# Performance work log

Measured on AMD Instinct MI355X. Metric: run time of the kernel, lower is better.

Reference implementation:

```python
import jax, jax.numpy as jnp
import numpy as np
from jax import lax

B, H, W, C = 2, 256, 256, 180
WS, SH, NH = 8, 4, 6
HD = C // NH          # 30
N = WS * WS           # 64
NW = (H // WS) * (W // WS)
HID = 4 * C
SCALE = HD ** -0.5
EPS = 1e-5


def _rel_pos_index(ws):
    coords = np.stack(np.meshgrid(np.arange(ws), np.arange(ws), indexing='ij'))  # [2,ws,ws]
    cf = coords.reshape(2, -1)
    rel = (cf[:, :, None] - cf[:, None, :]).transpose(1, 2, 0)  # [N,N,2]
    rel[:, :, 0] += ws - 1
    rel[:, :, 1] += ws - 1
    rel[:, :, 0] *= 2 * ws - 1
    return rel.sum(-1)  # [N,N]


def _attn_mask(h, w, ws, sh):
    img = np.zeros((h, w))
    sl = (slice(0, -ws), slice(-ws, -sh), slice(-sh, None))
    cnt = 0
    for hs in sl:
        for wsl in sl:
            img[hs, wsl] = cnt
            cnt += 1
    mw = img.reshape(h // ws, ws, w // ws, ws).transpose(0, 2, 1, 3).reshape(-1, ws * ws)  # [nW,N]
    d = mw[:, None, :] - mw[:, :, None]  # [nW,N,N]
    return np.where(d != 0, -100.0, 0.0).astype(np.float32)


REL_IDX = jnp.asarray(_rel_pos_index(WS))          # [N,N] int
MASK = jnp.asarray(_attn_mask(H, W, WS, SH))       # [nW,N,N] float


def _ln(x, g, b):
    m = jnp.mean(x, -1, keepdims=True)
    v = jnp.mean((x - m) ** 2, -1, keepdims=True)
    return (x - m) * lax.rsqrt(v + EPS) * g + b


def _win_part(x):  # (B,H,W,C) -> (B*nW,N,C)
    x = x.reshape(B, H // WS, WS, W // WS, WS, C).transpose(0, 1, 3, 2, 4, 5)
    return x.reshape(-1, N, C)


def _win_rev(w):  # (B*nW,N,C) -> (B,H,W,C)
    x = w.reshape(B, H // WS, W // WS, WS, WS, C).transpose(0, 1, 3, 2, 4, 5)
    return x.reshape(B, H, W, C)


def setup_inputs() -> dict:
    key = jax.random.key(0)
    ks = jax.random.split(key, 8)
    s = 0.02
    return {
        'x': jax.random.normal(ks[0], (B, H * W, C), jnp.float32),
        'norm1_g': jnp.ones((C,), jnp.float32),
        'norm1_b': jnp.zeros((C,), jnp.float32),
        'qkv_w': jax.random.normal(ks[1], (C, 3 * C), jnp.float32) * s,
        'qkv_b': jnp.zeros((3 * C,), jnp.float32),
        'rel_pos_table': jax.random.normal(ks[2], ((2 * WS - 1) ** 2, NH), jnp.float32) * s,
        'proj_w': jax.random.normal(ks[3], (C, C), jnp.float32) * s,
        'proj_b': jnp.zeros((C,), jnp.float32),
        'norm2_g': jnp.ones((C,), jnp.float32),
        'norm2_b': jnp.zeros((C,), jnp.float32),
        'fc1_w': jax.random.normal(ks[4], (C, HID), jnp.float32) * s,
        'fc1_b': jnp.zeros((HID,), jnp.float32),
        'dw_w': jax.random.normal(ks[5], (HID, 1, 3, 3), jnp.float32) * s,
        'dw_b': jnp.zeros((HID,), jnp.float32),
        'fc2_w': jax.random.normal(ks[6], (HID, C), jnp.float32) * s,
        'fc2_b': jnp.zeros((C,), jnp.float32),
    }


def reference(x, norm1_g, norm1_b, qkv_w, qkv_b, rel_pos_table, proj_w, proj_b,
              norm2_g, norm2_b, fc1_w, fc1_b, dw_w, dw_b, fc2_w, fc2_b):
    shortcut = x
    h = _ln(x, norm1_g, norm1_b).reshape(B, H, W, C)
    h = jnp.roll(h, (-SH, -SH), axis=(1, 2))           # cyclic shift
    xw = _win_part(h)                                   # [B*nW, N, C]

    qkv = (xw @ qkv_w + qkv_b).reshape(-1, N, 3, NH, HD).transpose(2, 0, 3, 1, 4)
    q, k, v = qkv[0] * SCALE, qkv[1], qkv[2]            # [B_,NH,N,HD]
    attn = jnp.einsum('bhnd,bhmd->bhnm', q, k)          # [B_,NH,N,N]

    bias = rel_pos_table[REL_IDX.reshape(-1)].reshape(N, N, NH).transpose(2, 0, 1)
    attn = attn + bias[None]
    attn = attn.reshape(B, NW, NH, N, N) + MASK[None, :, None]
    attn = jax.nn.softmax(attn.reshape(-1, NH, N, N), axis=-1)

    out = jnp.einsum('bhnm,bhmd->bhnd', attn, v).transpose(0, 2, 1, 3).reshape(-1, N, C)
    out = out @ proj_w + proj_b
    out = jnp.roll(_win_rev(out), (SH, SH), axis=(1, 2)).reshape(B, H * W, C)
    x = shortcut + out

    # MLP with depthwise-conv interleave
    m = _ln(x, norm2_g, norm2_b)
    m = jax.nn.gelu(m @ fc1_w + fc1_b, approximate=False)   # [B,L,HID]
    mc = m.transpose(0, 2, 1).reshape(B, HID, H, W)
    mc = lax.conv_general_dilated(mc, dw_w, (1, 1), 'SAME',
                                  feature_group_count=HID,
                                  dimension_numbers=('NCHW', 'OIHW', 'NCHW'))
    mc = mc + dw_b[None, :, None, None]
    m = jax.nn.gelu(mc.reshape(B, HID, H * W).transpose(0, 2, 1), approximate=False)
    m = m @ fc2_w + fc2_b
    return x + m
```

## Files before the change

kernel.cpp:

```cpp
#include <hip/hip_runtime.h>
#include <hip/hip_bf16.h>


using short8 = __attribute__((ext_vector_type(8))) short;
using f32x4  = __attribute__((ext_vector_type(4))) float;

constexpr int   ROWS   = 131072;
constexpr float SCALE_ = 0.18257418583505536f;

constexpr size_t OFF_WQ    = 0;
constexpr size_t OFF_WP    = OFF_WQ   + 576*192*2;
constexpr size_t OFF_WF1   = OFF_WP   + 192*192*2;
constexpr size_t OFF_WF2T  = OFF_WF1  + 768*192*2;
constexpr size_t OFF_BQ    = OFF_WF2T + 192*768*2;
constexpr size_t OFF_BP    = OFF_BQ   + 576*4;
constexpr size_t OFF_BF1   = OFF_BP   + 192*4;
constexpr size_t OFF_BF2   = OFF_BF1  + 768*4;
constexpr size_t OFF_BIASF = OFF_BF2  + 192*4;
constexpr size_t OFF_WDWT  = OFF_BIASF + 6*4096*4;
constexpr size_t OFF_BDW   = OFF_WDWT + 9*768*4;
constexpr size_t OFF_R1    = 1048576;
constexpr size_t SZ_R      = (size_t)ROWS * 192 * 2;
constexpr size_t OFF_R2    = OFF_R1 + SZ_R;
constexpr size_t OFF_R3    = OFF_R2 + SZ_R;
constexpr size_t WS_NEEDED = OFF_R3 + SZ_R;
static_assert(OFF_BDW + 768*4 <= OFF_R1, "weights overlap R1");
static_assert((size_t)66*256*768*2 <= SZ_R, "m1 band overflows R2");

__device__ __forceinline__ unsigned short f2bf(float f) {
    __hip_bfloat16 h = __float2bfloat16(f);
    return *reinterpret_cast<unsigned short*>(&h);
}
__device__ __forceinline__ float bf2f(unsigned short u) {
    union { unsigned int i; float f; } x; x.i = ((unsigned int)u) << 16; return x.f;
}
__device__ __forceinline__ float gelu_f(float x) {
    return 0.5f * x * (1.0f + erff(x * 0.70710678118654752f));
}

__global__ __launch_bounds__(256) void prep_kernel(
    const float* __restrict__ qkv_w, const float* __restrict__ qkv_b,
    const float* __restrict__ proj_w, const float* __restrict__ proj_b,
    const float* __restrict__ fc1_w, const float* __restrict__ fc1_b,
    const float* __restrict__ fc2_w, const float* __restrict__ fc2_b,
    const float* __restrict__ rpt,
    const float* __restrict__ dw_w, const float* __restrict__ dw_b,
    unsigned short* __restrict__ wq, unsigned short* __restrict__ wp,
    unsigned short* __restrict__ wf1, unsigned short* __restrict__ wf2t,
    float* __restrict__ bq, float* __restrict__ bp,
    float* __restrict__ bf1, float* __restrict__ bf2,
    float* __restrict__ biasf,
    float* __restrict__ wdwT, float* __restrict__ bdw)
{
    int idx = blockIdx.x * 256 + threadIdx.x;
    constexpr int E1 = 576*192;
    constexpr int E2 = E1 + 192*192;
    constexpr int E3 = E2 + 768*192;
    constexpr int E4 = E3 + 192*768;
    constexpr int E5 = E4 + 576;
    constexpr int E6 = E5 + 192;
    constexpr int E7 = E6 + 768;
    constexpr int E8 = E7 + 192;
    constexpr int E9 = E8 + 6*4096;
    constexpr int E10 = E9 + 9*768;
    constexpr int E11 = E10 + 768;
    if (idx < E1) {
        int n = idx / 192, kx = idx % 192;
        float v = 0.f;
        if (n < 540 && kx < 180) { v = qkv_w[kx*540 + n]; if (n < 180) v *= SCALE_; }
        wq[idx] = f2bf(v);
    } else if (idx < E2) {
        int j = idx - E1; int n = j / 192, kx = j % 192;
        wp[j] = f2bf((n < 180 && kx < 180) ? proj_w[kx*180 + n] : 0.f);
    } else if (idx < E3) {
        int j = idx - E2; int n = j / 192, kx = j % 192;
        wf1[j] = f2bf((n < 720 && kx < 180) ? fc1_w[kx*720 + n] : 0.f);
    } else if (idx < E4) {
        int j = idx - E3; int n = j / 768, kx = j % 768;
        wf2t[j] = f2bf((n < 180 && kx < 720) ? fc2_w[kx*180 + n] : 0.f);
    } else if (idx < E5) {
        int n = idx - E4;
        float v = (n < 540) ? qkv_b[n] : 0.f; if (n < 180) v *= SCALE_;
        bq[n] = v;
    } else if (idx < E6) {
        int n = idx - E5; bp[n] = (n < 180) ? proj_b[n] : 0.f;
    } else if (idx < E7) {
        int n = idx - E6; bf1[n] = (n < 720) ? fc1_b[n] : 0.f;
    } else if (idx < E8) {
        int n = idx - E7; bf2[n] = (n < 180) ? fc2_b[n] : 0.f;
    } else if (idx < E9) {
        int j = idx - E8;
        int hh = j / 4096, t = j & 4095;
        int n = t >> 6, m = t & 63;
        int rid = ((n>>3) - (m>>3) + 7)*15 + ((n&7) - (m&7) + 7);
        biasf[j] = rpt[rid*6 + hh];
    } else if (idx < E10) {
        int j = idx - E9;
        int tap = j / 768, c = j % 768;
        wdwT[j] = (c < 720) ? dw_w[c*9 + tap] : 0.f;
    } else if (idx < E11) {
        int c = idx - E10;
        bdw[c] = (c < 720) ? dw_b[c] : 0.f;
    }
}

template<int ROLL>
__global__ __launch_bounds__(256) void ln_kernel(const float* __restrict__ x,
    const float* __restrict__ g, const float* __restrict__ bsh,
    unsigned short* __restrict__ out)
{
    int row  = blockIdx.x * 4 + (threadIdx.x >> 6);
    int lane = threadIdx.x & 63;
    size_t src;
    if (ROLL) {
        int b    = row >> 16;
        int widx = (row >> 6) & 1023;
        int n    = row & 63;
        int hr   = ((widx >> 5) << 3) + (n >> 3);
        int wr   = ((widx & 31) << 3) + (n & 7);
        int h2   = (hr + 4) & 255;
        int w2   = (wr + 4) & 255;
        src = ((size_t)b << 16) + (h2 << 8) + w2;
    } else {
        src = (size_t)row;
    }
    const float* xr = x + src * 180;
    float v1 = xr[lane];
    float v2 = xr[lane + 64];
    float v3 = (lane < 52) ? xr[lane + 128] : 0.0f;
    float s1 = v1 + v2 + v3;
    float s2 = v1*v1 + v2*v2 + v3*v3;
    #pragma unroll
    for (int o = 32; o > 0; o >>= 1) { s1 += __shfl_xor(s1, o); s2 += __shfl_xor(s2, o); }
    float mean = s1 * (1.0f/180.0f);
    float var  = s2 * (1.0f/180.0f) - mean*mean;
    float rstd = rsqrtf(var + 1e-5f);
    unsigned short* orow = out + (size_t)row * 192;
    orow[lane]      = f2bf((v1 - mean)*rstd*g[lane]      + bsh[lane]);
    orow[lane + 64] = f2bf((v2 - mean)*rstd*g[lane + 64] + bsh[lane + 64]);
    if (lane < 52) orow[lane + 128] = f2bf((v3 - mean)*rstd*g[lane + 128] + bsh[lane + 128]);
    else           orow[lane + 128] = 0;
}

__global__ __launch_bounds__(256) void zeropad_kernel(unsigned int* q, unsigned int* k, unsigned int* v)
{
    int idx = blockIdx.x * 256 + threadIdx.x;
    int wid = idx / 192, t = idx % 192;
    if (t < 64)       q[wid*1024 + t*16 + 15] = 0;
    else if (t < 128) k[wid*1024 + (t-64)*16 + 15] = 0;
    else              v[wid*1024 + 960 + (t-128)] = 0;
}

template<int MODE>
__global__ __launch_bounds__(256) void gemm64(
    const unsigned short* __restrict__ A, const unsigned short* __restrict__ Bt,
    const float* __restrict__ bias, int K, int lda, int ldb, int ldo,
    float* __restrict__ out_f, const float* __restrict__ xres,
    unsigned short* __restrict__ oq, unsigned short* __restrict__ ok2,
    unsigned short* __restrict__ ov, unsigned short* __restrict__ obf)
{
    __shared__ __align__(16) unsigned short As[64*40];
    __shared__ __align__(16) unsigned short Bs[64*40];
    const int tid  = threadIdx.x;
    const int bm   = blockIdx.x, bn = blockIdx.y;
    const int lane = tid & 63;
    const int wv   = tid >> 6;
    const int wr   = wv >> 1, wc = wv & 1;
    const int l15  = lane & 15, l4 = lane >> 4;
    const int r    = tid >> 2;
    const int kk   = (tid & 3) << 3;

    f32x4 acc[2][2];
    #pragma unroll
    for (int i = 0; i < 2; i++)
        #pragma unroll
        for (int j = 0; j < 2; j++) acc[i][j] = f32x4{0.f, 0.f, 0.f, 0.f};

    const size_t abase = (size_t)(bm*64 + r) * (size_t)lda + kk;
    const size_t bbase = (size_t)(bn*64 + r) * (size_t)ldb + kk;
    const int lds_wi = r*40 + kk;

    for (int kt = 0; kt < K; kt += 32) {
        *(uint4*)&As[lds_wi] = *(const uint4*)&A[abase + kt];
        *(uint4*)&Bs[lds_wi] = *(const uint4*)&Bt[bbase + kt];
        __syncthreads();
        short8 af[2], bf[2];
        #pragma unroll
        for (int fm = 0; fm < 2; fm++) af[fm] = *(const short8*)&As[(wr*32 + fm*16 + l15)*40 + l4*8];
        #pragma unroll
        for (int fn = 0; fn < 2; fn++) bf[fn] = *(const short8*)&Bs[(wc*32 + fn*16 + l15)*40 + l4*8];
        #pragma unroll
        for (int fm = 0; fm < 2; fm++)
            #pragma unroll
            for (int fn = 0; fn < 2; fn++)
                acc[fm][fn] = __builtin_amdgcn_mfma_f32_16x16x32_bf16(af[fm], bf[fn], acc[fm][fn], 0, 0, 0);
        __syncthreads();
    }

    #pragma unroll
    for (int fm = 0; fm < 2; fm++) {
      #pragma unroll
      for (int fn = 0; fn < 2; fn++) {
        #pragma unroll
        for (int rr = 0; rr < 4; rr++) {
            int row_l = wr*32 + fm*16 + l4*4 + rr;
            int col_l = wc*32 + fn*16 + l15;
            int grow  = bm*64 + row_l;
            int gcol  = bn*64 + col_l;
            float v = acc[fm][fn][rr] + bias[gcol];
            if (MODE == 0) {
                if (gcol < 540) {
                    int which = (gcol >= 360) ? 2 : (gcol >= 180 ? 1 : 0);
                    int cc = gcol - which*180;
                    int hh = cc / 30;
                    int dd = cc - hh*30;
                    size_t wid = (size_t)(grow >> 6)*6 + hh;
                    if (which == 0)      oq [wid*2048 + (grow & 63)*32 + dd] = f2bf(v);
                    else if (which == 1) ok2[wid*2048 + (grow & 63)*32 + dd] = f2bf(v);
                    else                 ov [wid*2048 + dd*64 + (grow & 63)] = f2bf(v);
                }
            } else if (MODE == 1) {
                if (gcol < 180) {
                    int b    = grow >> 16;
                    int widx = (grow >> 6) & 1023;
                    int n    = grow & 63;
                    int hr   = ((widx >> 5) << 3) + (n >> 3);
                    int wr2  = ((widx & 31) << 3) + (n & 7);
                    int h2   = (hr + 4) & 255;
                    int w2   = (wr2 + 4) & 255;
                    size_t orow = ((size_t)b << 16) + (h2 << 8) + w2;
                    out_f[orow*180 + gcol] = xres[orow*180 + gcol] + v;
                }
            } else if (MODE == 2) {
                obf[(size_t)grow*ldo + gcol] = f2bf(gelu_f(v));
            } else {
                if (gcol < 180) out_f[(size_t)grow*180 + gcol] += v;
            }
        }
      }
    }
}

__global__ __launch_bounds__(64) void attn_kernel(
    const unsigned short* __restrict__ q, const unsigned short* __restrict__ k,
    const unsigned short* __restrict__ vt, const float* __restrict__ biasf,
    unsigned short* __restrict__ aout)
{
    __shared__ __align__(16) unsigned short P[64*72];
    const int wid  = blockIdx.x;
    const int b_   = wid / 6, hh = wid % 6;
    const int lane = threadIdx.x;
    const int l15  = lane & 15, l4 = lane >> 4;

    const unsigned short* qb = q  + (size_t)wid*2048;
    const unsigned short* kb = k  + (size_t)wid*2048;
    const unsigned short* vb = vt + (size_t)wid*2048;

    short8 qf[4], kf[4];
    #pragma unroll
    for (int t = 0; t < 4; t++) {
        qf[t] = *(const short8*)&qb[(t*16 + l15)*32 + l4*8];
        kf[t] = *(const short8*)&kb[(t*16 + l15)*32 + l4*8];
    }
    f32x4 s[4][4];
    #pragma unroll
    for (int m = 0; m < 4; m++)
        #pragma unroll
        for (int n = 0; n < 4; n++)
            s[m][n] = __builtin_amdgcn_mfma_f32_16x16x32_bf16(qf[m], kf[n], f32x4{0.f,0.f,0.f,0.f}, 0, 0, 0);

    const int wi = b_ & 1023;
    const int wh = wi >> 5, ww = wi & 31;
    const bool edge = (wh == 31) || (ww == 31);
    const float* bh = biasf + hh*4096;
    #pragma unroll
    for (int m = 0; m < 4; m++) {
      #pragma unroll
      for (int rr = 0; rr < 4; rr++) {
        int ni = m*16 + l4*4 + rr;
        int ln_n = 0;
        if (edge) {
            int rh = (wh < 31) ? 0 : (((ni >> 3) < 4) ? 1 : 2);
            int rw = (ww < 31) ? 0 : (((ni & 7) < 4) ? 1 : 2);
            ln_n = rh*3 + rw;
        }
        #pragma unroll
        for (int n = 0; n < 4; n++) {
            int mj = n*16 + l15;
            float add = bh[ni*64 + mj];
            if (edge) {
                int rh = (wh < 31) ? 0 : (((mj >> 3) < 4) ? 1 : 2);
                int rw = (ww < 31) ? 0 : (((mj & 7) < 4) ? 1 : 2);
                if (rh*3 + rw != ln_n) add -= 100.0f;
            }
            s[m][n][rr] += add;
        }
      }
    }
    #pragma unroll
    for (int m = 0; m < 4; m++) {
      #pragma unroll
      for (int rr = 0; rr < 4; rr++) {
        float mx = fmaxf(fmaxf(s[m][0][rr], s[m][1][rr]), fmaxf(s[m][2][rr], s[m][3][rr]));
        #pragma unroll
        for (int o = 8; o > 0; o >>= 1) mx = fmaxf(mx, __shfl_xor(mx, o));
        float sum = 0.f;
        #pragma unroll
        for (int n = 0; n < 4; n++) { float e = __expf(s[m][n][rr] - mx); s[m][n][rr] = e; sum += e; }
        #pragma unroll
        for (int o = 8; o > 0; o >>= 1) sum += __shfl_xor(sum, o);
        float inv = 1.0f / sum;
        int ni = m*16 + l4*4 + rr;
        #pragma unroll
        for (int n = 0; n < 4; n++) P[ni*72 + n*16 + l15] = f2bf(s[m][n][rr] * inv);
      }
    }
    __syncthreads();
    f32x4 po[4][2];
    #pragma unroll
    for (int m = 0; m < 4; m++)
        #pragma unroll
        for (int n = 0; n < 2; n++) po[m][n] = f32x4{0.f,0.f,0.f,0.f};
    #pragma unroll
    for (int ks = 0; ks < 2; ks++) {
        short8 pf[4], vf[2];
        #pragma unroll
        for (int m = 0; m < 4; m++) pf[m] = *(const short8*)&P[(m*16 + l15)*72 + ks*32 + l4*8];
        #pragma unroll
        for (int n = 0; n < 2; n++) vf[n] = *(const short8*)&vb[(n*16 + l15)*64 + ks*32 + l4*8];
        #pragma unroll
        for (int m = 0; m < 4; m++)
            #pragma unroll
            for (int n = 0; n < 2; n++)
                po[m][n] = __builtin_amdgcn_mfma_f32_16x16x32_bf16(pf[m], vf[n], po[m][n], 0, 0, 0);
    }
    #pragma unroll
    for (int m = 0; m < 4; m++)
      #pragma unroll
      for (int n = 0; n < 2; n++)
        #pragma unroll
        for (int rr = 0; rr < 4; rr++) {
            int ni = m*16 + l4*4 + rr;
            int dd = n*16 + l15;
            if (dd < 30)
                aout[((size_t)b_*64 + ni)*192 + hh*30 + dd] = f2bf(po[m][n][rr]);
        }
}

__global__ __launch_bounds__(256) void dwconv_band(
    const unsigned short* __restrict__ m1, const float* __restrict__ wT,
    const float* __restrict__ bias, int h0, unsigned short* __restrict__ m2)
{
    const int hl  = blockIdx.x;
    const int t   = threadIdx.x;
    const int cg  = t & 31;
    const int pl  = t >> 5;
    const int w0  = blockIdx.y * 64 + pl * 8;
    const int c   = blockIdx.z * 256 + cg * 8;

    float acc[8][8];
    float bv[8];
    *(f32x4*)&bv[0] = *(const f32x4*)&bias[c];
    *(f32x4*)&bv[4] = *(const f32x4*)&bias[c + 4];
    #pragma unroll
    for (int p = 0; p < 8; p++)
        #pragma unroll
        for (int i = 0; i < 8; i++) acc[p][i] = bv[i];

    const short8 zv = {0,0,0,0,0,0,0,0};
    #pragma unroll
    for (int dh = -1; dh <= 1; dh++) {
        int hg = h0 + hl + dh;
        if (hg < 0 || hg > 255) continue;
        const unsigned short* rb = m1 + (size_t)(hl + 1 + dh) * 256 * 768 + c;
        float f[10][8];
        #pragma unroll
        for (int j = 0; j < 10; j++) {
            int w2 = w0 - 1 + j;
            short8 v = (w2 < 0 || w2 > 255) ? zv : *(const short8*)&rb[(size_t)w2*768];
            #pragma unroll
            for (int i = 0; i < 8; i++) f[j][i] = bf2f((unsigned short)v[i]);
        }
        #pragma unroll
        for (int dw2 = 0; dw2 < 3; dw2++) {
            const float* wrow = wT + ((dh+1)*3 + dw2)*768 + c;
            float wt[8];
            *(f32x4*)&wt[0] = *(const f32x4*)&wrow[0];
            *(f32x4*)&wt[4] = *(const f32x4*)&wrow[4];
            #pragma unroll
            for (int p = 0; p < 8; p++)
                #pragma unroll
                for (int i = 0; i < 8; i++)
                    acc[p][i] += f[p + dw2][i] * wt[i];
        }
    }
    unsigned short* ob = m2 + ((size_t)hl*256 + w0)*768 + c;
    #pragma unroll
    for (int p = 0; p < 8; p++) {
        short8 o;
        #pragma unroll
        for (int i = 0; i < 8; i++) o[i] = (short)f2bf(gelu_f(acc[p][i]));
        *(short8*)&ob[(size_t)p*768] = o;
    }
}

extern "C" void kernel_launch(void* const* d_in, const int* in_sizes, int n_in,
                              void* d_out, int out_size, void* d_ws, size_t ws_size,
                              hipStream_t stream) {
    (void)in_sizes; (void)n_in; (void)out_size;
    if (ws_size < WS_NEEDED) return;
    const float* x      = (const float*)d_in[0];
    const float* n1g    = (const float*)d_in[1];
    const float* n1b    = (const float*)d_in[2];
    const float* qkv_w  = (const float*)d_in[3];
    const float* qkv_b  = (const float*)d_in[4];
    const float* rpt    = (const float*)d_in[5];
    const float* proj_w = (const float*)d_in[6];
    const float* proj_b = (const float*)d_in[7];
    const float* n2g    = (const float*)d_in[8];
    const float* n2b    = (const float*)d_in[9];
    const float* fc1_w  = (const float*)d_in[10];
    const float* fc1_b  = (const float*)d_in[11];
    const float* dw_w   = (const float*)d_in[12];
    const float* dw_b   = (const float*)d_in[13];
    const float* fc2_w  = (const float*)d_in[14];
    const float* fc2_b  = (const float*)d_in[15];
    float* out = (float*)d_out;
    char*  ws  = (char*)d_ws;

    unsigned short* wq   = (unsigned short*)(ws + OFF_WQ);
    unsigned short* wp   = (unsigned short*)(ws + OFF_WP);
    unsigned short* wf1  = (unsigned short*)(ws + OFF_WF1);
    unsigned short* wf2t = (unsigned short*)(ws + OFF_WF2T);
    float* bq    = (float*)(ws + OFF_BQ);
    float* bp    = (float*)(ws + OFF_BP);
    float* bf1   = (float*)(ws + OFF_BF1);
    float* bf2   = (float*)(ws + OFF_BF2);
    float* biasf = (float*)(ws + OFF_BIASF);
    float* wdwT  = (float*)(ws + OFF_WDWT);
    float* bdw   = (float*)(ws + OFF_BDW);
    unsigned short* R1 = (unsigned short*)(ws + OFF_R1);
    unsigned short* R2 = (unsigned short*)(ws + OFF_R2);
    unsigned short* R3 = (unsigned short*)(ws + OFF_R3);
    unsigned short* qp = (unsigned short*)d_out;

    prep_kernel<<<1861, 256, 0, stream>>>(qkv_w, qkv_b, proj_w, proj_b, fc1_w, fc1_b,
                                          fc2_w, fc2_b, rpt, dw_w, dw_b,
                                          wq, wp, wf1, wf2t,
                                          bq, bp, bf1, bf2, biasf, wdwT, bdw);
    ln_kernel<1><<<32768, 256, 0, stream>>>(x, n1g, n1b, R1);
    gemm64<0><<<dim3(2048, 9), 256, 0, stream>>>(R1, wq, bq, 192, 192, 192, 0,
                                                 nullptr, nullptr, qp, R2, R3, nullptr);
    zeropad_kernel<<<9216, 256, 0, stream>>>((unsigned int*)qp, (unsigned int*)R2, (unsigned int*)R3);
    attn_kernel<<<12288, 64, 0, stream>>>(qp, R2, R3, biasf, R1);
    gemm64<1><<<dim3(2048, 3), 256, 0, stream>>>(R1, wp, bp, 192, 192, 192, 0,
                                                 out, x, nullptr, nullptr, nullptr, nullptr);
    ln_kernel<0><<<32768, 256, 0, stream>>>(out, n2g, n2b, R1);
    for (int band = 0; band < 8; ++band) {
        const int b_img   = band >> 2;
        const int h0      = (band & 3) * 64;
        const int h_start = (h0 == 0) ? 0 : h0 - 1;
        const int h_end   = (h0 + 64 < 256) ? (h0 + 65) : 256;
        const int n_rows  = h_end - h_start;
        const int moff    = (h0 == 0) ? 1 : 0;
        const size_t arow0 = ((size_t)b_img*256 + h_start) * 256;
        const size_t pix0  = ((size_t)b_img*256 + h0) * 256;
        gemm64<2><<<dim3(n_rows*4, 12), 256, 0, stream>>>(
            R1 + arow0*192, wf1, bf1, 192, 192, 192, 768,
            nullptr, nullptr, nullptr, nullptr, nullptr, R2 + (size_t)moff*256*768);
        dwconv_band<<<dim3(64, 4, 3), 256, 0, stream>>>(R2, wdwT, bdw, h0, R3);
        gemm64<3><<<dim3(256, 3), 256, 0, stream>>>(
            R3, wf2t, bf2, 768, 768, 768, 0,
            out + pix0*180, nullptr, nullptr, nullptr, nullptr, nullptr);
    }
}
```

Baseline: 897.7 us.

## Fuse LN1, QKV GEMM, window attention and projection into one per-window kernel

Replaces the separate roll+LayerNorm, QKV GEMM, zero-pad, attention and projection kernels with one kernel per window. Each block holds the normalized tokens, Q/K/V, the probabilities and the attention output in LDS. This removes the global round trips for the bf16 intermediates and several launches. The cost is about 113KB of LDS and 384 threads per block, so only one block fits per CU. The QKV and projection weights are also read straight from global memory by every block.

```diff
diff --git a/kernel.cpp b/kernel.cpp
--- a/kernel.cpp
+++ b/kernel.cpp
@@ -104,27 +104,13 @@
     }
 }
 
-template<int ROLL>
 __global__ __launch_bounds__(256) void ln_kernel(const float* __restrict__ x,
     const float* __restrict__ g, const float* __restrict__ bsh,
     unsigned short* __restrict__ out)
 {
     int row  = blockIdx.x * 4 + (threadIdx.x >> 6);
     int lane = threadIdx.x & 63;
-    size_t src;
-    if (ROLL) {
-        int b    = row >> 16;
-        int widx = (row >> 6) & 1023;
-        int n    = row & 63;
-        int hr   = ((widx >> 5) << 3) + (n >> 3);
-        int wr   = ((widx & 31) << 3) + (n & 7);
-        int h2   = (hr + 4) & 255;
-        int w2   = (wr + 4) & 255;
-        src = ((size_t)b << 16) + (h2 << 8) + w2;
-    } else {
-        src = (size_t)row;
-    }
-    const float* xr = x + src * 180;
+    const float* xr = x + (size_t)row * 180;
     float v1 = xr[lane];
     float v2 = xr[lane + 64];
     float v3 = (lane < 52) ? xr[lane + 128] : 0.0f;
@@ -142,22 +128,249 @@
     else           orow[lane + 128] = 0;
 }
 
-__global__ __launch_bounds__(256) void zeropad_kernel(unsigned int* q, unsigned int* k, unsigned int* v)
+__global__ __launch_bounds__(384, 1) void fused_attn(
+    const float* __restrict__ x,
+    const float* __restrict__ n1g, const float* __restrict__ n1b,
+    const unsigned short* __restrict__ wq, const float* __restrict__ bq,
+    const unsigned short* __restrict__ wp, const float* __restrict__ bp,
+    const float* __restrict__ biasf, float* __restrict__ out)
 {
-    int idx = blockIdx.x * 256 + threadIdx.x;
-    int wid = idx / 192, t = idx % 192;
-    if (t < 64)       q[wid*1024 + t*16 + 15] = 0;
-    else if (t < 128) k[wid*1024 + (t-64)*16 + 15] = 0;
-    else              v[wid*1024 + 960 + (t-128)] = 0;
+    __shared__ __align__(16) char lds[115712];
+    unsigned short* xn  = (unsigned short*)(lds);
+    unsigned short* qs  = (unsigned short*)(lds + 26624);
+    unsigned short* ks  = (unsigned short*)(lds + 57344);
+    unsigned short* vsT = (unsigned short*)(lds + 88064);
+    unsigned short* P   = (unsigned short*)(lds);
+    unsigned short* ao  = (unsigned short*)(lds + 88064);
+
+    const int wid  = blockIdx.x;
+    const int b_   = wid >> 10;
+    const int wi   = wid & 1023;
+    const int wh   = wi >> 5, ww = wi & 31;
+    const int tid  = threadIdx.x;
+    const int wv   = tid >> 6;
+    const int lane = tid & 63;
+    const int l15  = lane & 15, l4 = lane >> 4;
+
+    for (int n = wv; n < 64; n += 6) {
+        int h2 = (wh*8 + (n >> 3) + 4) & 255;
+        int w2 = (ww*8 + (n & 7) + 4) & 255;
+        const float* xr = x + ((size_t)(b_ << 16) + (h2 << 8) + w2) * 180;
+        float v1 = xr[lane];
+        float v2 = xr[lane + 64];
+        float v3 = (lane < 52) ? xr[lane + 128] : 0.0f;
+        float s1 = v1 + v2 + v3;
+        float s2 = v1*v1 + v2*v2 + v3*v3;
+        #pragma unroll
+        for (int o = 32; o > 0; o >>= 1) { s1 += __shfl_xor(s1, o); s2 += __shfl_xor(s2, o); }
+        float mean = s1 * (1.0f/180.0f);
+        float var  = s2 * (1.0f/180.0f) - mean*mean;
+        float rstd = rsqrtf(var + 1e-5f);
+        unsigned short* orow = xn + n*208;
+        orow[lane]      = f2bf((v1 - mean)*rstd*n1g[lane]      + n1b[lane]);
+        orow[lane + 64] = f2bf((v2 - mean)*rstd*n1g[lane + 64] + n1b[lane + 64]);
+        if (lane < 52) orow[lane + 128] = f2bf((v3 - mean)*rstd*n1g[lane + 128] + n1b[lane + 128]);
+        else           orow[lane + 128] = 0;
+    }
+    {
+        int hh = tid >> 6, tk = tid & 63;
+        *(unsigned int*)&qs[(hh*64 + tk)*40 + 30] = 0;
+        *(unsigned int*)&ks[(hh*64 + tk)*40 + 30] = 0;
+    }
+    __syncthreads();
+
+    {
+        f32x4 acc[4][6];
+        #pragma unroll
+        for (int m = 0; m < 4; m++)
+            #pragma unroll
+            for (int nb = 0; nb < 6; nb++) acc[m][nb] = f32x4{0.f,0.f,0.f,0.f};
+        for (int kt = 0; kt < 6; kt++) {
+            short8 af[4];
+            #pragma unroll
+            for (int m = 0; m < 4; m++)
+                af[m] = *(const short8*)&xn[(m*16 + l15)*208 + kt*32 + l4*8];
+            #pragma unroll
+            for (int nb = 0; nb < 6; nb++) {
+                short8 bf = *(const short8*)&wq[(size_t)(wv*96 + nb*16 + l15)*192 + kt*32 + l4*8];
+                #pragma unroll
+                for (int m = 0; m < 4; m++)
+                    acc[m][nb] = __builtin_amdgcn_mfma_f32_16x16x32_bf16(af[m], bf, acc[m][nb], 0, 0, 0);
+            }
+        }
+        #pragma unroll
+        for (int m = 0; m < 4; m++) {
+          #pragma unroll
+          for (int nb = 0; nb < 6; nb++) {
+            #pragma unroll
+            for (int rr = 0; rr < 4; rr++) {
+                int tok  = m*16 + l4*4 + rr;
+                int gcol = wv*96 + nb*16 + l15;
+                if (gcol < 540) {
+                    float v = acc[m][nb][rr] + bq[gcol];
+                    int which = (gcol >= 360) ? 2 : (gcol >= 180 ? 1 : 0);
+                    int cc = gcol - which*180;
+                    int hh = cc / 30;
+                    int dd = cc - hh*30;
+                    if (which == 0)      qs [(hh*64 + tok)*40 + dd] = f2bf(v);
+                    else if (which == 1) ks [(hh*64 + tok)*40 + dd] = f2bf(v);
+                    else                 vsT[(hh*32 + dd)*72 + tok] = f2bf(v);
+                }
+            }
+          }
+        }
+    }
+    __syncthreads();
+
+    const int hh = wv;
+    f32x4 s[4][4];
+    {
+        short8 qf[4], kf[4];
+        #pragma unroll
+        for (int t = 0; t < 4; t++) {
+            qf[t] = *(const short8*)&qs[(hh*64 + t*16 + l15)*40 + l4*8];
+            kf[t] = *(const short8*)&ks[(hh*64 + t*16 + l15)*40 + l4*8];
+        }
+        #pragma unroll
+        for (int m = 0; m < 4; m++)
+            #pragma unroll
+            for (int n = 0; n < 4; n++)
+                s[m][n] = __builtin_amdgcn_mfma_f32_16x16x32_bf16(qf[m], kf[n], f32x4{0.f,0.f,0.f,0.f}, 0, 0, 0);
+    }
+    const bool edge = (wh == 31) || (ww == 31);
+    const float* bh = biasf + hh*4096;
+    #pragma unroll
+    for (int m = 0; m < 4; m++) {
+      #pragma unroll
+      for (int rr = 0; rr < 4; rr++) {
+        int ni = m*16 + l4*4 + rr;
+        int ln_n = 0;
+        if (edge) {
+            int rh = (wh < 31) ? 0 : (((ni >> 3) < 4) ? 1 : 2);
+            int rw = (ww < 31) ? 0 : (((ni & 7) < 4) ? 1 : 2);
+            ln_n = rh*3 + rw;
+        }
+        #pragma unroll
+        for (int n = 0; n < 4; n++) {
+            int mj = n*16 + l15;
+            float add = bh[ni*64 + mj];
+            if (edge) {
+                int rh = (wh < 31) ? 0 : (((mj >> 3) < 4) ? 1 : 2);
+                int rw = (ww < 31) ? 0 : (((mj & 7) < 4) ? 1 : 2);
+                if (rh*3 + rw != ln_n) add -= 100.0f;
+            }
+            s[m][n][rr] += add;
+        }
+      }
+    }
+    #pragma unroll
+    for (int m = 0; m < 4; m++) {
+      #pragma unroll
+      for (int rr = 0; rr < 4; rr++) {
+        float mx = fmaxf(fmaxf(s[m][0][rr], s[m][1][rr]), fmaxf(s[m][2][rr], s[m][3][rr]));
+        #pragma unroll
+        for (int o = 8; o > 0; o >>= 1) mx = fmaxf(mx, __shfl_xor(mx, o));
+        float sum = 0.f;
+        #pragma unroll
+        for (int n = 0; n < 4; n++) { float e = __expf(s[m][n][rr] - mx); s[m][n][rr] = e; sum += e; }
+        #pragma unroll
+        for (int o = 8; o > 0; o >>= 1) sum += __shfl_xor(sum, o);
+        float inv = 1.0f / sum;
+        #pragma unroll
+        for (int n = 0; n < 4; n++) s[m][n][rr] *= inv;
+      }
+    }
+    __syncthreads();
+
+    #pragma unroll
+    for (int m = 0; m < 4; m++)
+      #pragma unroll
+      for (int rr = 0; rr < 4; rr++) {
+        int ni = m*16 + l4*4 + rr;
+        #pragma unroll
+        for (int n = 0; n < 4; n++) P[(hh*64 + ni)*72 + n*16 + l15] = f2bf(s[m][n][rr]);
+      }
+    f32x4 po[4][2];
+    #pragma unroll
+    for (int m = 0; m < 4; m++)
+        #pragma unroll
+        for (int n = 0; n < 2; n++) po[m][n] = f32x4{0.f,0.f,0.f,0.f};
+    #pragma unroll
+    for (int ksx = 0; ksx < 2; ksx++) {
+        short8 pf[4], vf[2];
+        #pragma unroll
+        for (int m = 0; m < 4; m++) pf[m] = *(const short8*)&P[(hh*64 + m*16 + l15)*72 + ksx*32 + l4*8];
+        #pragma unroll
+        for (int n = 0; n < 2; n++) vf[n] = *(const short8*)&vsT[(hh*32 + n*16 + l15)*72 + ksx*32 + l4*8];
+        #pragma unroll
+        for (int m = 0; m < 4; m++)
+            #pragma unroll
+            for (int n = 0; n < 2; n++)
+                po[m][n] = __builtin_amdgcn_mfma_f32_16x16x32_bf16(pf[m], vf[n], po[m][n], 0, 0, 0);
+    }
+    __syncthreads();
+
+    #pragma unroll
+    for (int m = 0; m < 4; m++)
+      #pragma unroll
+      for (int n = 0; n < 2; n++)
+        #pragma unroll
+        for (int rr = 0; rr < 4; rr++) {
+            int tok = m*16 + l4*4 + rr;
+            int dd  = n*16 + l15;
+            if (dd < 30) ao[tok*208 + hh*30 + dd] = f2bf(po[m][n][rr]);
+        }
+    if (wv == 0) {
+        #pragma unroll
+        for (int c = 0; c < 6; c++)
+            *(unsigned int*)&ao[lane*208 + 180 + c*2] = 0;
+    }
+    __syncthreads();
+
+    {
+        f32x4 pacc[4][2];
+        #pragma unroll
+        for (int m = 0; m < 4; m++)
+            #pragma unroll
+            for (int nb = 0; nb < 2; nb++) pacc[m][nb] = f32x4{0.f,0.f,0.f,0.f};
+        for (int kt = 0; kt < 6; kt++) {
+            short8 paf[4];
+            #pragma unroll
+            for (int m = 0; m < 4; m++)
+                paf[m] = *(const short8*)&ao[(m*16 + l15)*208 + kt*32 + l4*8];
+            #pragma unroll
+            for (int nb = 0; nb < 2; nb++) {
+                short8 pbf = *(const short8*)&wp[(size_t)(wv*32 + nb*16 + l15)*192 + kt*32 + l4*8];
+                #pragma unroll
+                for (int m = 0; m < 4; m++)
+                    pacc[m][nb] = __builtin_amdgcn_mfma_f32_16x16x32_bf16(paf[m], pbf, pacc[m][nb], 0, 0, 0);
+            }
+        }
+        #pragma unroll
+        for (int m = 0; m < 4; m++) {
+          #pragma unroll
+          for (int nb = 0; nb < 2; nb++) {
+            int gcol = wv*32 + nb*16 + l15;
+            if (gcol < 180) {
+              #pragma unroll
+              for (int rr = 0; rr < 4; rr++) {
+                int tok = m*16 + l4*4 + rr;
+                int h2  = (wh*8 + (tok >> 3) + 4) & 255;
+                int w2  = (ww*8 + (tok & 7) + 4) & 255;
+                size_t orow = ((size_t)b_ << 16) + (h2 << 8) + w2;
+                out[orow*180 + gcol] = x[orow*180 + gcol] + pacc[m][nb][rr] + bp[gcol];
+              }
+            }
+          }
+        }
+    }
 }
 
 template<int MODE>
 __global__ __launch_bounds__(256) void gemm64(
     const unsigned short* __restrict__ A, const unsigned short* __restrict__ Bt,
     const float* __restrict__ bias, int K, int lda, int ldb, int ldo,
-    float* __restrict__ out_f, const float* __restrict__ xres,
-    unsigned short* __restrict__ oq, unsigned short* __restrict__ ok2,
-    unsigned short* __restrict__ ov, unsigned short* __restrict__ obf)
+    float* __restrict__ out_f, unsigned short* __restrict__ obf)
 {
     __shared__ __align__(16) unsigned short As[64*40];
     __shared__ __align__(16) unsigned short Bs[64*40];
@@ -203,35 +416,10 @@
       for (int fn = 0; fn < 2; fn++) {
         #pragma unroll
         for (int rr = 0; rr < 4; rr++) {
-            int row_l = wr*32 + fm*16 + l4*4 + rr;
-            int col_l = wc*32 + fn*16 + l15;
-            int grow  = bm*64 + row_l;
-            int gcol  = bn*64 + col_l;
+            int grow  = bm*64 + wr*32 + fm*16 + l4*4 + rr;
+            int gcol  = bn*64 + wc*32 + fn*16 + l15;
             float v = acc[fm][fn][rr] + bias[gcol];
-            if (MODE == 0) {
-                if (gcol < 540) {
-                    int which = (gcol >= 360) ? 2 : (gcol >= 180 ? 1 : 0);
-                    int cc = gcol - which*180;
-                    int hh = cc / 30;
-                    int dd = cc - hh*30;
-                    size_t wid = (size_t)(grow >> 6)*6 + hh;
-                    if (which == 0)      oq [wid*2048 + (grow & 63)*32 + dd] = f2bf(v);
-                    else if (which == 1) ok2[wid*2048 + (grow & 63)*32 + dd] = f2bf(v);
-                    else                 ov [wid*2048 + dd*64 + (grow & 63)] = f2bf(v);
-                }
-            } else if (MODE == 1) {
-                if (gcol < 180) {
-                    int b    = grow >> 16;
-                    int widx = (grow >> 6) & 1023;
-                    int n    = grow & 63;
-                    int hr   = ((widx >> 5) << 3) + (n >> 3);
-                    int wr2  = ((widx & 31) << 3) + (n & 7);
-                    int h2   = (hr + 4) & 255;
-                    int w2   = (wr2 + 4) & 255;
-                    size_t orow = ((size_t)b << 16) + (h2 << 8) + w2;
-                    out_f[orow*180 + gcol] = xres[orow*180 + gcol] + v;
-                }
-            } else if (MODE == 2) {
+            if (MODE == 2) {
                 obf[(size_t)grow*ldo + gcol] = f2bf(gelu_f(v));
             } else {
                 if (gcol < 180) out_f[(size_t)grow*180 + gcol] += v;
@@ -239,112 +427,6 @@
         }
       }
     }
-}
-
-__global__ __launch_bounds__(64) void attn_kernel(
-    const unsigned short* __restrict__ q, const unsigned short* __restrict__ k,
-    const unsigned short* __restrict__ vt, const float* __restrict__ biasf,
-    unsigned short* __restrict__ aout)
-{
-    __shared__ __align__(16) unsigned short P[64*72];
-    const int wid  = blockIdx.x;
-    const int b_   = wid / 6, hh = wid % 6;
-    const int lane = threadIdx.x;
-    const int l15  = lane & 15, l4 = lane >> 4;
-
-    const unsigned short* qb = q  + (size_t)wid*2048;
-    const unsigned short* kb = k  + (size_t)wid*2048;
-    const unsigned short* vb = vt + (size_t)wid*2048;
-
-    short8 qf[4], kf[4];
-    #pragma unroll
-    for (int t = 0; t < 4; t++) {
-        qf[t] = *(const short8*)&qb[(t*16 + l15)*32 + l4*8];
-        kf[t] = *(const short8*)&kb[(t*16 + l15)*32 + l4*8];
-    }
-    f32x4 s[4][4];
-    #pragma unroll
-    for (int m = 0; m < 4; m++)
-        #pragma unroll
-        for (int n = 0; n < 4; n++)
-            s[m][n] = __builtin_amdgcn_mfma_f32_16x16x32_bf16(qf[m], kf[n], f32x4{0.f,0.f,0.f,0.f}, 0, 0, 0);
-
-    const int wi = b_ & 1023;
-    const int wh = wi >> 5, ww = wi & 31;
-    const bool edge = (wh == 31) || (ww == 31);
-    const float* bh = biasf + hh*4096;
-    #pragma unroll
-    for (int m = 0; m < 4; m++) {
-      #pragma unroll
-      for (int rr = 0; rr < 4; rr++) {
-        int ni = m*16 + l4*4 + rr;
-        int ln_n = 0;
-        if (edge) {
-            int rh = (wh < 31) ? 0 : (((ni >> 3) < 4) ? 1 : 2);
-            int rw = (ww < 31) ? 0 : (((ni & 7) < 4) ? 1 : 2);
-            ln_n = rh*3 + rw;
-        }
-        #pragma unroll
-        for (int n = 0; n < 4; n++) {
-            int mj = n*16 + l15;
-            float add = bh[ni*64 + mj];
-            if (edge) {
-                int rh = (wh < 31) ? 0 : (((mj >> 3) < 4) ? 1 : 2);
-                int rw = (ww < 31) ? 0 : (((mj & 7) < 4) ? 1 : 2);
-                if (rh*3 + rw != ln_n) add -= 100.0f;
-            }
-            s[m][n][rr] += add;
-        }
-      }
-    }
-    #pragma unroll
-    for (int m = 0; m < 4; m++) {
-      #pragma unroll
-      for (int rr = 0; rr < 4; rr++) {
-        float mx = fmaxf(fmaxf(s[m][0][rr], s[m][1][rr]), fmaxf(s[m][2][rr], s[m][3][rr]));
-        #pragma unroll
-        for (int o = 8; o > 0; o >>= 1) mx = fmaxf(mx, __shfl_xor(mx, o));
-        float sum = 0.f;
-        #pragma unroll
-        for (int n = 0; n < 4; n++) { float e = __expf(s[m][n][rr] - mx); s[m][n][rr] = e; sum += e; }
-        #pragma unroll
-        for (int o = 8; o > 0; o >>= 1) sum += __shfl_xor(sum, o);
-        float inv = 1.0f / sum;
-        int ni = m*16 + l4*4 + rr;
-        #pragma unroll
-        for (int n = 0; n < 4; n++) P[ni*72 + n*16 + l15] = f2bf(s[m][n][rr] * inv);
-      }
-    }
-    __syncthreads();
-    f32x4 po[4][2];
-    #pragma unroll
-    for (int m = 0; m < 4; m++)
-        #pragma unroll
-        for (int n = 0; n < 2; n++) po[m][n] = f32x4{0.f,0.f,0.f,0.f};
-    #pragma unroll
-    for (int ks = 0; ks < 2; ks++) {
-        short8 pf[4], vf[2];
-        #pragma unroll
-        for (int m = 0; m < 4; m++) pf[m] = *(const short8*)&P[(m*16 + l15)*72 + ks*32 + l4*8];
-        #pragma unroll
-        for (int n = 0; n < 2; n++) vf[n] = *(const short8*)&vb[(n*16 + l15)*64 + ks*32 + l4*8];
-        #pragma unroll
-        for (int m = 0; m < 4; m++)
-            #pragma unroll
-            for (int n = 0; n < 2; n++)
-                po[m][n] = __builtin_amdgcn_mfma_f32_16x16x32_bf16(pf[m], vf[n], po[m][n], 0, 0, 0);
-    }
-    #pragma unroll
-    for (int m = 0; m < 4; m++)
-      #pragma unroll
-      for (int n = 0; n < 2; n++)
-        #pragma unroll
-        for (int rr = 0; rr < 4; rr++) {
-            int ni = m*16 + l4*4 + rr;
-            int dd = n*16 + l15;
-            if (dd < 30)
-                aout[((size_t)b_*64 + ni)*192 + hh*30 + dd] = f2bf(po[m][n][rr]);
-        }
 }
 
 __global__ __launch_bounds__(256) void dwconv_band(
@@ -442,20 +524,13 @@
     unsigned short* R1 = (unsigned short*)(ws + OFF_R1);
     unsigned short* R2 = (unsigned short*)(ws + OFF_R2);
     unsigned short* R3 = (unsigned short*)(ws + OFF_R3);
-    unsigned short* qp = (unsigned short*)d_out;
 
     prep_kernel<<<1861, 256, 0, stream>>>(qkv_w, qkv_b, proj_w, proj_b, fc1_w, fc1_b,
                                           fc2_w, fc2_b, rpt, dw_w, dw_b,
                                           wq, wp, wf1, wf2t,
                                           bq, bp, bf1, bf2, biasf, wdwT, bdw);
-    ln_kernel<1><<<32768, 256, 0, stream>>>(x, n1g, n1b, R1);
-    gemm64<0><<<dim3(2048, 9), 256, 0, stream>>>(R1, wq, bq, 192, 192, 192, 0,
-                                                 nullptr, nullptr, qp, R2, R3, nullptr);
-    zeropad_kernel<<<9216, 256, 0, stream>>>((unsigned int*)qp, (unsigned int*)R2, (unsigned int*)R3);
-    attn_kernel<<<12288, 64, 0, stream>>>(qp, R2, R3, biasf, R1);
-    gemm64<1><<<dim3(2048, 3), 256, 0, stream>>>(R1, wp, bp, 192, 192, 192, 0,
-                                                 out, x, nullptr, nullptr, nullptr, nullptr);
-    ln_kernel<0><<<32768, 256, 0, stream>>>(out, n2g, n2b, R1);
+    fused_attn<<<2048, 384, 0, stream>>>(x, n1g, n1b, wq, bq, wp, bp, biasf, out);
+    ln_kernel<<<32768, 256, 0, stream>>>(out, n2g, n2b, R1);
     for (int band = 0; band < 8; ++band) {
         const int b_img   = band >> 2;
         const int h0      = (band & 3) * 64;
@@ -467,10 +542,10 @@
         const size_t pix0  = ((size_t)b_img*256 + h0) * 256;
         gemm64<2><<<dim3(n_rows*4, 12), 256, 0, stream>>>(
             R1 + arow0*192, wf1, bf1, 192, 192, 192, 768,
-            nullptr, nullptr, nullptr, nullptr, nullptr, R2 + (size_t)moff*256*768);
+            nullptr, R2 + (size_t)moff*256*768);
         dwconv_band<<<dim3(64, 4, 3), 256, 0, stream>>>(R2, wdwT, bdw, h0, R3);
         gemm64<3><<<dim3(256, 3), 256, 0, stream>>>(
             R3, wf2t, bf2, 768, 768, 768, 0,
-            out + pix0*180, nullptr, nullptr, nullptr, nullptr, nullptr);
-    }
-}
+            out + pix0*180, nullptr);
+    }
+}
```

New measurement: 867.8 us. 3.3% less time.

## Add full-width N=192 GEMM with LDS-staged vectorized epilogue for proj and fc2

Applied to the files above, without the earlier changes.

Adds a gemmN192 kernel in which each block computes all 192 output columns, so the A tile is loaded once per block instead of once per N-tile. The kernel stages results in LDS so the fp32 residual writes are coalesced and vectorized. It replaces the proj (with window reverse, shift and residual) and fc2 (accumulate) paths. It also swaps the grid order of the remaining gemm64 launches so that blocks sharing an A tile are scheduled next to each other. The cost is larger LDS use and fewer blocks, and fc2 now uses 32-row tiles with a 768-long K loop.

```diff
diff --git a/kernel.cpp b/kernel.cpp
--- a/kernel.cpp
+++ b/kernel.cpp
@@ -155,14 +155,13 @@
 __global__ __launch_bounds__(256) void gemm64(
     const unsigned short* __restrict__ A, const unsigned short* __restrict__ Bt,
     const float* __restrict__ bias, int K, int lda, int ldb, int ldo,
-    float* __restrict__ out_f, const float* __restrict__ xres,
     unsigned short* __restrict__ oq, unsigned short* __restrict__ ok2,
     unsigned short* __restrict__ ov, unsigned short* __restrict__ obf)
 {
     __shared__ __align__(16) unsigned short As[64*40];
     __shared__ __align__(16) unsigned short Bs[64*40];
     const int tid  = threadIdx.x;
-    const int bm   = blockIdx.x, bn = blockIdx.y;
+    const int bn   = blockIdx.x, bm = blockIdx.y;
     const int lane = tid & 63;
     const int wv   = tid >> 6;
     const int wr   = wv >> 1, wc = wv & 1;
@@ -203,10 +202,8 @@
       for (int fn = 0; fn < 2; fn++) {
         #pragma unroll
         for (int rr = 0; rr < 4; rr++) {
-            int row_l = wr*32 + fm*16 + l4*4 + rr;
-            int col_l = wc*32 + fn*16 + l15;
-            int grow  = bm*64 + row_l;
-            int gcol  = bn*64 + col_l;
+            int grow  = bm*64 + wr*32 + fm*16 + l4*4 + rr;
+            int gcol  = bn*64 + wc*32 + fn*16 + l15;
             float v = acc[fm][fn][rr] + bias[gcol];
             if (MODE == 0) {
                 if (gcol < 540) {
@@ -219,25 +216,109 @@
                     else if (which == 1) ok2[wid*2048 + (grow & 63)*32 + dd] = f2bf(v);
                     else                 ov [wid*2048 + dd*64 + (grow & 63)] = f2bf(v);
                 }
-            } else if (MODE == 1) {
-                if (gcol < 180) {
-                    int b    = grow >> 16;
-                    int widx = (grow >> 6) & 1023;
-                    int n    = grow & 63;
-                    int hr   = ((widx >> 5) << 3) + (n >> 3);
-                    int wr2  = ((widx & 31) << 3) + (n & 7);
-                    int h2   = (hr + 4) & 255;
-                    int w2   = (wr2 + 4) & 255;
-                    size_t orow = ((size_t)b << 16) + (h2 << 8) + w2;
-                    out_f[orow*180 + gcol] = xres[orow*180 + gcol] + v;
-                }
-            } else if (MODE == 2) {
+            } else {
                 obf[(size_t)grow*ldo + gcol] = f2bf(gelu_f(v));
-            } else {
-                if (gcol < 180) out_f[(size_t)grow*180 + gcol] += v;
             }
         }
       }
+    }
+}
+
+template<int M_BLK, int MODE>
+__global__ __launch_bounds__(256) void gemmN192(
+    const unsigned short* __restrict__ A, const unsigned short* __restrict__ Bt,
+    const float* __restrict__ bias, int K, int lda, int ldb,
+    const float* __restrict__ xres, float* __restrict__ out)
+{
+    constexpr int MB = M_BLK / 16;
+    constexpr int LDS_STAGE = (M_BLK*40 + 192*40) * 2;
+    constexpr int LDS_CST   = M_BLK * 180 * 4;
+    constexpr int LDSZ = LDS_STAGE > LDS_CST ? LDS_STAGE : LDS_CST;
+    __shared__ __align__(16) char lds[LDSZ];
+    unsigned short* As = (unsigned short*)lds;
+    unsigned short* Bs = As + M_BLK*40;
+    float* Cst = (float*)lds;
+
+    const int tid  = threadIdx.x;
+    const int bm   = blockIdx.x;
+    const int lane = tid & 63;
+    const int wv   = tid >> 6;
+    const int l15  = lane & 15, l4 = lane >> 4;
+    const int r    = tid >> 2;
+    const int kk   = (tid & 3) << 3;
+
+    f32x4 acc[MB][3];
+    #pragma unroll
+    for (int m = 0; m < MB; m++)
+        #pragma unroll
+        for (int nb = 0; nb < 3; nb++) acc[m][nb] = f32x4{0.f,0.f,0.f,0.f};
+
+    const size_t abase = (size_t)(bm*M_BLK + r) * (size_t)lda + kk;
+    const size_t bbase = (size_t)r * (size_t)ldb + kk;
+
+    for (int kt = 0; kt < K; kt += 32) {
+        if (M_BLK == 64 || tid < M_BLK*4)
+            *(uint4*)&As[r*40 + kk] = *(const uint4*)&A[abase + kt];
+        #pragma unroll
+        for (int jj = 0; jj < 3; jj++)
+            *(uint4*)&Bs[(r + jj*64)*40 + kk] = *(const uint4*)&Bt[bbase + (size_t)jj*64*ldb + kt];
+        __syncthreads();
+        short8 af[MB], bf[3];
+        #pragma unroll
+        for (int m = 0; m < MB; m++) af[m] = *(const short8*)&As[(m*16 + l15)*40 + l4*8];
+        #pragma unroll
+        for (int nb = 0; nb < 3; nb++) bf[nb] = *(const short8*)&Bs[(wv*48 + nb*16 + l15)*40 + l4*8];
+        #pragma unroll
+        for (int m = 0; m < MB; m++)
+            #pragma unroll
+            for (int nb = 0; nb < 3; nb++)
+                acc[m][nb] = __builtin_amdgcn_mfma_f32_16x16x32_bf16(af[m], bf[nb], acc[m][nb], 0, 0, 0);
+        __syncthreads();
+    }
+
+    #pragma unroll
+    for (int m = 0; m < MB; m++)
+      #pragma unroll
+      for (int nb = 0; nb < 3; nb++)
+        #pragma unroll
+        for (int rr = 0; rr < 4; rr++) {
+            int tok = m*16 + l4*4 + rr;
+            int col = wv*48 + nb*16 + l15;
+            if (col < 180) Cst[tok*180 + col] = acc[m][nb][rr];
+        }
+    __syncthreads();
+
+    for (int idx = tid; idx < M_BLK*4; idx += 256) {
+        int tok = idx >> 2, j = idx & 3;
+        int c0  = j * 48;
+        int cnt = (j == 3) ? 36 : 48;
+        size_t orow;
+        if (MODE == 0) {
+            int grow = bm*M_BLK + tok;
+            int wig  = grow >> 6;
+            int b_   = wig >> 10, wi = wig & 1023, ti = grow & 63;
+            int h2   = (((wi >> 5) << 3) + (ti >> 3) + 4) & 255;
+            int w2   = (((wi & 31) << 3) + (ti & 7) + 4) & 255;
+            orow = ((size_t)b_ << 16) + (h2 << 8) + w2;
+        } else {
+            orow = (size_t)(bm*M_BLK + tok);
+        }
+        float*       op = out  + orow*180 + c0;
+        const float* cp = &Cst[tok*180 + c0];
+        const float* bb = bias + c0;
+        if (MODE == 0) {
+            const float* xp = xres + orow*180 + c0;
+            for (int i = 0; i < cnt; i += 4) {
+                f32x4 ov = *(const f32x4*)&xp[i] + *(const f32x4*)&cp[i] + *(const f32x4*)&bb[i];
+                *(f32x4*)&op[i] = ov;
+            }
+        } else {
+            for (int i = 0; i < cnt; i += 4) {
+                f32x4 ov = *(const f32x4*)&op[i];
+                ov += *(const f32x4*)&cp[i] + *(const f32x4*)&bb[i];
+                *(f32x4*)&op[i] = ov;
+            }
+        }
     }
 }
 
@@ -449,12 +530,11 @@
                                           wq, wp, wf1, wf2t,
                                           bq, bp, bf1, bf2, biasf, wdwT, bdw);
     ln_kernel<1><<<32768, 256, 0, stream>>>(x, n1g, n1b, R1);
-    gemm64<0><<<dim3(2048, 9), 256, 0, stream>>>(R1, wq, bq, 192, 192, 192, 0,
-                                                 nullptr, nullptr, qp, R2, R3, nullptr);
+    gemm64<0><<<dim3(9, 2048), 256, 0, stream>>>(R1, wq, bq, 192, 192, 192, 0,
+                                                 qp, R2, R3, nullptr);
     zeropad_kernel<<<9216, 256, 0, stream>>>((unsigned int*)qp, (unsigned int*)R2, (unsigned int*)R3);
     attn_kernel<<<12288, 64, 0, stream>>>(qp, R2, R3, biasf, R1);
-    gemm64<1><<<dim3(2048, 3), 256, 0, stream>>>(R1, wp, bp, 192, 192, 192, 0,
-                                                 out, x, nullptr, nullptr, nullptr, nullptr);
+    gemmN192<64, 0><<<2048, 256, 0, stream>>>(R1, wp, bp, 192, 192, 192, x, out);
     ln_kernel<0><<<32768, 256, 0, stream>>>(out, n2g, n2b, R1);
     for (int band = 0; band < 8; ++band) {
         const int b_img   = band >> 2;
@@ -465,12 +545,11 @@
         const int moff    = (h0 == 0) ? 1 : 0;
         const size_t arow0 = ((size_t)b_img*256 + h_start) * 256;
         const size_t pix0  = ((size_t)b_img*256 + h0) * 256;
-        gemm64<2><<<dim3(n_rows*4, 12), 256, 0, stream>>>(
+        gemm64<2><<<dim3(12, n_rows*4), 256, 0, stream>>>(
             R1 + arow0*192, wf1, bf1, 192, 192, 192, 768,
-            nullptr, nullptr, nullptr, nullptr, nullptr, R2 + (size_t)moff*256*768);
+            nullptr, nullptr, nullptr, R2 + (size_t)moff*256*768);
         dwconv_band<<<dim3(64, 4, 3), 256, 0, stream>>>(R2, wdwT, bdw, h0, R3);
-        gemm64<3><<<dim3(256, 3), 256, 0, stream>>>(
-            R3, wf2t, bf2, 768, 768, 768, 0,
-            out + pix0*180, nullptr, nullptr, nullptr, nullptr, nullptr);
-    }
-}
+        gemmN192<32, 1><<<512, 256, 0, stream>>>(
+            R3, wf2t, bf2, 768, 768, 768, nullptr, out + pix0*180);
+    }
+}
```

Measured after the change: 936.6 us. +4.3%, slower.
